# Performance work log

Hardware: AMD Instinct MI355X
Metric: run time of the kernel (lower is better)

The kernel has to match this reference:

```python
import jax, jax.numpy as jnp
import numpy as np

DT, TAU = 0.02, 0.1


def setup_inputs() -> dict:
    key = jax.random.key(0)
    ks = jax.random.split(key, 7)
    B, T, IN, H = 64, 2048, 64, 256
    return {
        "x0": jax.random.normal(ks[0], (B, H), jnp.float32),
        "I": jax.random.normal(ks[1], (B, T, IN), jnp.float32),
        "W_in": jax.random.normal(ks[2], (H, IN), jnp.float32) / np.sqrt(IN),
        "W_rec": jax.random.normal(ks[3], (H, H), jnp.float32) / np.sqrt(H),
        "b": jax.random.normal(ks[4], (H,), jnp.float32) * 0.1,
        "Wout": jax.random.normal(ks[5], (2, H), jnp.float32) / np.sqrt(H),
        "bout": jax.random.normal(ks[6], (2,), jnp.float32) * 0.1,
    }


def reference(x0, I, W_in, W_rec, b, Wout, bout):
    # Continuous-time leaky RNN, forward-Euler integration.
    # u_{t+1} = (1 - dt/tau) * u_t + (dt/tau) * (tanh(u_t) @ W_rec^T + I_t @ W_in^T + b)
    alpha = DT / TAU

    def step(u, I_t):
        r = jnp.tanh(u)                                   # [B, H]
        drive = r @ W_rec.T + I_t @ W_in.T + b            # [B, H]
        u_new = (1.0 - alpha) * u + alpha * drive
        return u_new, u_new

    I_tbf = jnp.swapaxes(I, 0, 1)                         # [T, B, IN]
    _, us = jax.lax.scan(step, x0, I_tbf)                 # [T, B, H]
    u = jnp.swapaxes(us, 0, 1)                            # [B, T, H]
    y = u @ Wout.T + bout                                 # [B, T, 2] linear readout
    return u, y
```

## Files before the change

kernel.cpp:

```cpp
#include <hip/hip_runtime.h>

#define BB 64
#define TT 2048
#define INW 64
#define HH 256

typedef float v2f __attribute__((ext_vector_type(2)));

__device__ __forceinline__ v2f fma2(v2f a, v2f b, v2f c) {
#if __has_builtin(__builtin_elementwise_fma)
    return __builtin_elementwise_fma(a, b, c);
#else
    v2f r; r.x = __builtin_fmaf(a.x, b.x, c.x); r.y = __builtin_fmaf(a.y, b.y, c.y); return r;
#endif
}

__device__ __forceinline__ float fast_tanh(float x) {
    float e = __expf(2.0f * x);
    return 1.0f - 2.0f / (e + 1.0f);
}

__device__ __forceinline__ void lds_barrier() {
    asm volatile("s_waitcnt lgkmcnt(0)" ::: "memory");
    __builtin_amdgcn_s_barrier();
    __builtin_amdgcn_sched_barrier(0);
}

__global__ __launch_bounds__(512, 1)
void rnn_scan(const float* __restrict__ x0,
              const float* __restrict__ I,
              const float* __restrict__ W_in,
              const float* __restrict__ W_rec,
              const float* __restrict__ bias,
              float* __restrict__ u_out)
{
    __shared__ __align__(16) float r_buf[HH];
    __shared__ __align__(16) float i_buf[INW];
    __shared__ float part[4][HH + 1];

    const int b   = blockIdx.x;
    const int tid = threadIdx.x;
    const int h2  = tid & 127;
    const int q   = tid >> 7;
    const int k0  = q * 64;
    const int j0  = q * 16;
    const int hA  = h2;
    const int hB  = h2 + 128;

    v2f wrA[32], wrB[32], wiA[8], wiB[8];
    {
        const float4* wa = (const float4*)(W_rec + (size_t)hA * HH + k0);
        const float4* wb = (const float4*)(W_rec + (size_t)hB * HH + k0);
        #pragma unroll
        for (int i = 0; i < 16; ++i) {
            float4 a = wa[i], bq = wb[i];
            wrA[2*i]     = (v2f){a.x, a.y};  wrA[2*i + 1] = (v2f){a.z, a.w};
            wrB[2*i]     = (v2f){bq.x, bq.y}; wrB[2*i + 1] = (v2f){bq.z, bq.w};
        }
        const float4* ia = (const float4*)(W_in + (size_t)hA * INW + j0);
        const float4* ib = (const float4*)(W_in + (size_t)hB * INW + j0);
        #pragma unroll
        for (int i = 0; i < 4; ++i) {
            float4 a = ia[i], bq = ib[i];
            wiA[2*i]     = (v2f){a.x, a.y};  wiA[2*i + 1] = (v2f){a.z, a.w};
            wiB[2*i]     = (v2f){bq.x, bq.y}; wiB[2*i + 1] = (v2f){bq.z, bq.w};
        }
    }

    float u = 0.0f, bv = 0.0f;
    if (tid < HH) {
        u  = x0[(size_t)b * HH + tid];
        bv = bias[tid];
        r_buf[tid] = fast_tanh(u);
    }
    if (tid < INW) i_buf[tid] = I[((size_t)b * TT + 0) * INW + tid];
    __syncthreads();

    const float4* rb4 = (const float4*)&r_buf[k0];
    const float4* ib4 = (const float4*)&i_buf[j0];

    for (int t = 0; t < TT; ++t) {
        float i_next = 0.0f;
        if (tid < INW && (t + 1) < TT)
            i_next = I[((size_t)b * TT + (t + 1)) * INW + tid];

        v2f aA0 = {0.f,0.f}, aA1 = {0.f,0.f}, aB0 = {0.f,0.f}, aB1 = {0.f,0.f};
        #pragma unroll
        for (int i = 0; i < 16; ++i) {
            float4 r4 = rb4[i];
            v2f r01 = (v2f){r4.x, r4.y}, r23 = (v2f){r4.z, r4.w};
            aA0 = fma2(wrA[2*i],     r01, aA0);
            aA1 = fma2(wrA[2*i + 1], r23, aA1);
            aB0 = fma2(wrB[2*i],     r01, aB0);
            aB1 = fma2(wrB[2*i + 1], r23, aB1);
        }
        #pragma unroll
        for (int i = 0; i < 4; ++i) {
            float4 r4 = ib4[i];
            v2f r01 = (v2f){r4.x, r4.y}, r23 = (v2f){r4.z, r4.w};
            aA0 = fma2(wiA[2*i],     r01, aA0);
            aA1 = fma2(wiA[2*i + 1], r23, aA1);
            aB0 = fma2(wiB[2*i],     r01, aB0);
            aB1 = fma2(wiB[2*i + 1], r23, aB1);
        }
        v2f sA = aA0 + aA1, sB = aB0 + aB1;
        part[q][hA] = sA.x + sA.y;
        part[q][hB] = sB.x + sB.y;
        lds_barrier();

        if (tid < HH) {
            float d = ((part[0][tid] + part[1][tid]) + (part[2][tid] + part[3][tid])) + bv;
            u = 0.8f * u + 0.2f * d;
            u_out[((size_t)b * TT + t) * HH + tid] = u;
            r_buf[tid] = fast_tanh(u);
        }
        if (tid < INW) i_buf[tid] = i_next;
        lds_barrier();
    }
}

__global__ __launch_bounds__(256)
void readout(const float* __restrict__ u,
             const float* __restrict__ Wout,
             const float* __restrict__ bout,
             float* __restrict__ y)
{
    const int wid  = threadIdx.x >> 6;
    const int lane = threadIdx.x & 63;
    const size_t row = (size_t)blockIdx.x * 4 + wid;

    float4 uv = ((const float4*)(u + row * HH))[lane];
    float4 w0 = ((const float4*)Wout)[lane];
    float4 w1 = ((const float4*)(Wout + HH))[lane];

    float acc0 = uv.x * w0.x + uv.y * w0.y + uv.z * w0.z + uv.w * w0.w;
    float acc1 = uv.x * w1.x + uv.y * w1.y + uv.z * w1.z + uv.w * w1.w;

    #pragma unroll
    for (int m = 32; m >= 1; m >>= 1) {
        acc0 += __shfl_xor(acc0, m, 64);
        acc1 += __shfl_xor(acc1, m, 64);
    }
    if (lane == 0) {
        y[row * 2 + 0] = acc0 + bout[0];
        y[row * 2 + 1] = acc1 + bout[1];
    }
}

extern "C" void kernel_launch(void* const* d_in, const int* in_sizes, int n_in,
                              void* d_out, int out_size, void* d_ws, size_t ws_size,
                              hipStream_t stream) {
    const float* x0    = (const float*)d_in[0];
    const float* I     = (const float*)d_in[1];
    const float* W_in  = (const float*)d_in[2];
    const float* W_rec = (const float*)d_in[3];
    const float* bias  = (const float*)d_in[4];
    const float* Wout  = (const float*)d_in[5];
    const float* bout  = (const float*)d_in[6];

    float* u_out = (float*)d_out;
    float* y_out = u_out + (size_t)BB * TT * HH;

    rnn_scan<<<BB, 512, 0, stream>>>(x0, I, W_in, W_rec, bias, u_out);
    readout<<<(BB * TT) / 4, 256, 0, stream>>>(u_out, Wout, bout, y_out);
}
```

Before: 1.572 ms.

## Replace LDS partial-sum reduction with quad DPP reduction and double-buffered state

Reassigns threads so the four K-slices of each hidden unit sit in adjacent lanes, and reduces the partial dot products with DPP quad shuffles instead of writing them to shared memory. Every lane then computes the state update redundantly. The tanh state and input buffers are double-buffered with padded strides, which cuts the two barriers per timestep to one and removes the serial phase in which only 256 threads work. Input prefetch now runs two steps ahead. The cost is redundant update arithmetic on every lane and u_out stores issued from a strided lane subset, which coalesce less well.

```diff
diff --git a/kernel.cpp b/kernel.cpp
--- a/kernel.cpp
+++ b/kernel.cpp
@@ -4,6 +4,8 @@
 #define TT 2048
 #define INW 64
 #define HH 256
+#define RBW 68
+#define IBW 20
 
 typedef float v2f __attribute__((ext_vector_type(2)));
 
@@ -24,6 +26,13 @@
     asm volatile("s_waitcnt lgkmcnt(0)" ::: "memory");
     __builtin_amdgcn_s_barrier();
     __builtin_amdgcn_sched_barrier(0);
+}
+
+__device__ __forceinline__ float quad_xor1(float x) {
+    return __int_as_float(__builtin_amdgcn_mov_dpp(__float_as_int(x), 0xB1, 0xF, 0xF, true));
+}
+__device__ __forceinline__ float quad_xor2(float x) {
+    return __int_as_float(__builtin_amdgcn_mov_dpp(__float_as_int(x), 0x4E, 0xF, 0xF, true));
 }
 
 __global__ __launch_bounds__(512, 1)
@@ -34,18 +43,17 @@
               const float* __restrict__ bias,
               float* __restrict__ u_out)
 {
-    __shared__ __align__(16) float r_buf[HH];
-    __shared__ __align__(16) float i_buf[INW];
-    __shared__ float part[4][HH + 1];
+    __shared__ __align__(16) float rb[2][4 * RBW];
+    __shared__ __align__(16) float ibuf[2][4 * IBW];
 
     const int b   = blockIdx.x;
     const int tid = threadIdx.x;
-    const int h2  = tid & 127;
-    const int q   = tid >> 7;
+    const int q   = tid & 3;
+    const int rp  = tid >> 2;
+    const int hA  = rp;
+    const int hB  = rp + 128;
     const int k0  = q * 64;
     const int j0  = q * 16;
-    const int hA  = h2;
-    const int hB  = h2 + 128;
 
     v2f wrA[32], wrB[32], wiA[8], wiB[8];
     {
@@ -54,7 +62,7 @@
         #pragma unroll
         for (int i = 0; i < 16; ++i) {
             float4 a = wa[i], bq = wb[i];
-            wrA[2*i]     = (v2f){a.x, a.y};  wrA[2*i + 1] = (v2f){a.z, a.w};
+            wrA[2*i]     = (v2f){a.x, a.y};   wrA[2*i + 1] = (v2f){a.z, a.w};
             wrB[2*i]     = (v2f){bq.x, bq.y}; wrB[2*i + 1] = (v2f){bq.z, bq.w};
         }
         const float4* ia = (const float4*)(W_in + (size_t)hA * INW + j0);
@@ -62,59 +70,85 @@
         #pragma unroll
         for (int i = 0; i < 4; ++i) {
             float4 a = ia[i], bq = ib[i];
-            wiA[2*i]     = (v2f){a.x, a.y};  wiA[2*i + 1] = (v2f){a.z, a.w};
+            wiA[2*i]     = (v2f){a.x, a.y};   wiA[2*i + 1] = (v2f){a.z, a.w};
             wiB[2*i]     = (v2f){bq.x, bq.y}; wiB[2*i + 1] = (v2f){bq.z, bq.w};
         }
     }
 
-    float u = 0.0f, bv = 0.0f;
-    if (tid < HH) {
-        u  = x0[(size_t)b * HH + tid];
-        bv = bias[tid];
-        r_buf[tid] = fast_tanh(u);
-    }
-    if (tid < INW) i_buf[tid] = I[((size_t)b * TT + 0) * INW + tid];
+    float uA = x0[(size_t)b * HH + hA];
+    float uB = x0[(size_t)b * HH + hB];
+    const float bvA = bias[hA];
+    const float bvB = bias[hB];
+
+    const int rsA = RBW * (hA >> 6) + (hA & 63);
+    const int rsB = RBW * (hB >> 6) + (hB & 63);
+    const int iw  = IBW * (tid >> 2) + 4 * (tid & 3);
+
+    if (q == 0) {
+        rb[0][rsA] = fast_tanh(uA);
+        rb[0][rsB] = fast_tanh(uB);
+    }
+    float4 i_next = {0.f, 0.f, 0.f, 0.f};
+    if (tid < 16) {
+        float4 i0 = ((const float4*)(I + (size_t)b * TT * INW))[tid];
+        *(float4*)&ibuf[0][iw] = i0;
+        i_next = ((const float4*)(I + ((size_t)b * TT + 1) * INW))[tid];
+    }
     __syncthreads();
 
-    const float4* rb4 = (const float4*)&r_buf[k0];
-    const float4* ib4 = (const float4*)&i_buf[j0];
-
+    #pragma unroll 2
     for (int t = 0; t < TT; ++t) {
-        float i_next = 0.0f;
-        if (tid < INW && (t + 1) < TT)
-            i_next = I[((size_t)b * TT + (t + 1)) * INW + tid];
-
-        v2f aA0 = {0.f,0.f}, aA1 = {0.f,0.f}, aB0 = {0.f,0.f}, aB1 = {0.f,0.f};
+        const int p = t & 1;
+
+        float4 i_fut = {0.f, 0.f, 0.f, 0.f};
+        if (tid < 16 && (t + 2) < TT)
+            i_fut = ((const float4*)(I + ((size_t)b * TT + t + 2) * INW))[tid];
+
+        const float4* r4 = (const float4*)&rb[p][RBW * q];
+        const float4* i4 = (const float4*)&ibuf[p][IBW * q];
+
+        v2f a0 = {0.f,0.f}, a1 = {0.f,0.f}, c0 = {0.f,0.f}, c1 = {0.f,0.f};
         #pragma unroll
         for (int i = 0; i < 16; ++i) {
-            float4 r4 = rb4[i];
-            v2f r01 = (v2f){r4.x, r4.y}, r23 = (v2f){r4.z, r4.w};
-            aA0 = fma2(wrA[2*i],     r01, aA0);
-            aA1 = fma2(wrA[2*i + 1], r23, aA1);
-            aB0 = fma2(wrB[2*i],     r01, aB0);
-            aB1 = fma2(wrB[2*i + 1], r23, aB1);
+            float4 r = r4[i];
+            v2f r01 = (v2f){r.x, r.y}, r23 = (v2f){r.z, r.w};
+            a0 = fma2(wrA[2*i],     r01, a0);
+            a1 = fma2(wrA[2*i + 1], r23, a1);
+            c0 = fma2(wrB[2*i],     r01, c0);
+            c1 = fma2(wrB[2*i + 1], r23, c1);
         }
         #pragma unroll
         for (int i = 0; i < 4; ++i) {
-            float4 r4 = ib4[i];
-            v2f r01 = (v2f){r4.x, r4.y}, r23 = (v2f){r4.z, r4.w};
-            aA0 = fma2(wiA[2*i],     r01, aA0);
-            aA1 = fma2(wiA[2*i + 1], r23, aA1);
-            aB0 = fma2(wiB[2*i],     r01, aB0);
-            aB1 = fma2(wiB[2*i + 1], r23, aB1);
-        }
-        v2f sA = aA0 + aA1, sB = aB0 + aB1;
-        part[q][hA] = sA.x + sA.y;
-        part[q][hB] = sB.x + sB.y;
-        lds_barrier();
-
-        if (tid < HH) {
-            float d = ((part[0][tid] + part[1][tid]) + (part[2][tid] + part[3][tid])) + bv;
-            u = 0.8f * u + 0.2f * d;
-            u_out[((size_t)b * TT + t) * HH + tid] = u;
-            r_buf[tid] = fast_tanh(u);
-        }
-        if (tid < INW) i_buf[tid] = i_next;
+            float4 r = i4[i];
+            v2f r01 = (v2f){r.x, r.y}, r23 = (v2f){r.z, r.w};
+            a0 = fma2(wiA[2*i],     r01, a0);
+            a1 = fma2(wiA[2*i + 1], r23, a1);
+            c0 = fma2(wiB[2*i],     r01, c0);
+            c1 = fma2(wiB[2*i + 1], r23, c1);
+        }
+        v2f sA = a0 + a1, sB = c0 + c1;
+        float dA = sA.x + sA.y, dB = sB.x + sB.y;
+
+        dA += quad_xor1(dA);  dB += quad_xor1(dB);
+        dA += quad_xor2(dA);  dB += quad_xor2(dB);
+
+        uA = 0.8f * uA + 0.2f * (dA + bvA);
+        uB = 0.8f * uB + 0.2f * (dB + bvB);
+        float rA = fast_tanh(uA), rB = fast_tanh(uB);
+
+        if (q == 0) {
+            rb[p ^ 1][rsA] = rA;
+            rb[p ^ 1][rsB] = rB;
+        }
+        if (tid < 16 && (t + 1) < TT)
+            *(float4*)&ibuf[p ^ 1][iw] = i_next;
+        i_next = i_fut;
+        if (q == 1) {
+            float* uo = u_out + ((size_t)b * TT + t) * HH;
+            uo[hA] = uA;
+            uo[hB] = uB;
+        }
+
         lds_barrier();
     }
 }
```

Result: slower. 1.639 ms (+4.3%).
